# Kernel optimization log

Hardware: AMD Instinct MI355X
Metric: run time of the kernel (lower is better)

Reference implementation:

```python
import jax, jax.numpy as jnp
import numpy as np

HIDDEN = 1024
INTER = 256
N_EXPERTS = 16
B, T = 4, 2048
NEG_INF = -1000000000.0


def setup_inputs() -> dict:
    key = jax.random.key(0)
    ks = jax.random.split(key, 5)
    hidden_states = jax.random.normal(ks[0], (B, T, HIDDEN), dtype=jnp.float32)
    sim_matrix = jax.random.normal(ks[1], (HIDDEN, N_EXPERTS), dtype=jnp.float32)
    threshold = jnp.zeros((1,), dtype=jnp.float32)
    # torch Linear weights: w1 [I, C], w2 [C, I]; store per-expert stacked in
    # matmul-friendly layout: w1 [E, C, I], w2 [E, I, C]
    w1 = jax.random.normal(ks[2], (N_EXPERTS, HIDDEN, INTER), dtype=jnp.float32) / np.sqrt(HIDDEN)
    w2 = jax.random.normal(ks[3], (N_EXPERTS, INTER, HIDDEN), dtype=jnp.float32) / np.sqrt(INTER)
    return {"hidden_states": hidden_states, "sim_matrix": sim_matrix,
            "threshold": threshold, "w1": w1, "w2": w2}


def _l2norm(x, axis):
    return x / jnp.maximum(jnp.linalg.norm(x, axis=axis, keepdims=True), 1e-12)


def reference(hidden_states, sim_matrix, threshold, w1, w2):
    Bq, Tq, C = hidden_states.shape
    x = hidden_states.reshape(-1, C)                      # [N, C]
    # gate
    scores = _l2norm(x, -1) @ _l2norm(sim_matrix, 0)      # [N, E]
    activated = scores > threshold
    k_per_token = activated.sum(axis=-1)                  # [N] int
    masked = jnp.where(activated, scores, NEG_INF)
    routing_weights = jax.nn.softmax(masked, axis=-1)     # [N, E]
    # dense all-expert FFN
    h = jax.nn.gelu(jnp.einsum('nc,eci->nei', x, w1), approximate=False)
    out = jnp.einsum('nei,eic->nec', h, w2)               # [N, E, C]
    final = jnp.einsum('nec,ne->nc', out, routing_weights)
    return final.reshape(Bq, Tq, C), scores, k_per_token
```

## Files before the change

### kernel.cpp

```cpp
#include <hip/hip_runtime.h>
#include <hip/hip_bf16.h>
#include <math.h>

#define NTOK 8192
#define HID  1024
#define ISZ  256
#define NEXP 16
#define NBIG 4096

typedef __attribute__((ext_vector_type(8))) short bf16x8;
typedef __attribute__((ext_vector_type(4))) float f32x4;

__device__ __forceinline__ unsigned short f2bf(float f) {
  unsigned u = __float_as_uint(f);
  u += 0x7fff + ((u >> 16) & 1);
  return (unsigned short)(u >> 16);
}

__device__ __forceinline__ void async16(void* l, const void* g) {
  __builtin_amdgcn_global_load_lds(
      (const __attribute__((address_space(1))) unsigned int*)g,
      (__attribute__((address_space(3))) unsigned int*)l, 16, 0, 0);
}

__global__ void simnorm_kernel(const float* __restrict__ sm, float* __restrict__ inv_smn) {
  __shared__ float red[16][17];
  int t = threadIdx.x;
  int e = t & 15, g = t >> 4;
  float ss = 0.f;
  for (int c = g; c < HID; c += 16) {
    float v = sm[c * NEXP + e];
    ss += v * v;
  }
  red[e][g] = ss;
  __syncthreads();
  if (t < 16) {
    float s = 0.f;
    #pragma unroll
    for (int i = 0; i < 16; i++) s += red[t][i];
    inv_smn[t] = 1.f / fmaxf(sqrtf(s), 1e-12f);
  }
}

__global__ __launch_bounds__(256)
void gate_kernel(const float* __restrict__ x, const float* __restrict__ sm,
                 const float* __restrict__ thr, const float* __restrict__ inv_smn,
                 float* __restrict__ scores_out, float* __restrict__ k_out,
                 float* __restrict__ rw_out, unsigned short* __restrict__ xb_out) {
  const int n = blockIdx.x;
  const int t = threadIdx.x;
  const int lane = t & 63, wave = t >> 6;
  const float* xr = x + (size_t)n * HID;

  float p[16];
  #pragma unroll
  for (int e = 0; e < 16; e++) p[e] = 0.f;
  float ss = 0.f;

  #pragma unroll
  for (int q = 0; q < 4; q++) {
    int c = t + q * 256;
    float v = xr[c];
    ss += v * v;
    xb_out[(size_t)n * HID + c] = f2bf(v);
    const float4* smr = (const float4*)(sm + (size_t)c * NEXP);
    float4 s0 = smr[0], s1 = smr[1], s2 = smr[2], s3 = smr[3];
    p[0] += v * s0.x;  p[1] += v * s0.y;  p[2] += v * s0.z;  p[3] += v * s0.w;
    p[4] += v * s1.x;  p[5] += v * s1.y;  p[6] += v * s1.z;  p[7] += v * s1.w;
    p[8] += v * s2.x;  p[9] += v * s2.y;  p[10] += v * s2.z; p[11] += v * s2.w;
    p[12] += v * s3.x; p[13] += v * s3.y; p[14] += v * s3.z; p[15] += v * s3.w;
  }

  #pragma unroll
  for (int off = 32; off > 0; off >>= 1) {
    ss += __shfl_down(ss, off, 64);
    #pragma unroll
    for (int e = 0; e < 16; e++) p[e] += __shfl_down(p[e], off, 64);
  }

  __shared__ float red[4][17];
  __shared__ float sc[16];
  if (lane == 0) {
    red[wave][0] = ss;
    #pragma unroll
    for (int e = 0; e < 16; e++) red[wave][1 + e] = p[e];
  }
  __syncthreads();

  if (t < 16) {
    float d = red[0][1 + t] + red[1][1 + t] + red[2][1 + t] + red[3][1 + t];
    float ssum = red[0][0] + red[1][0] + red[2][0] + red[3][0];
    float inv_x = 1.f / fmaxf(sqrtf(ssum), 1e-12f);
    float s = d * inv_x * inv_smn[t];
    scores_out[(size_t)n * 16 + t] = s;
    sc[t] = s;
  }
  __syncthreads();

  if (t < 16) {
    float thrv = thr[0];
    float s = sc[t];
    bool act = s > thrv;
    float m = act ? s : -INFINITY;
    int cnt = act ? 1 : 0;
    #pragma unroll
    for (int off = 8; off > 0; off >>= 1) {
      m = fmaxf(m, __shfl_xor(m, off, 16));
      cnt += __shfl_xor(cnt, off, 16);
    }
    float pv;
    if (cnt > 0) pv = act ? expf(s - m) : 0.f;
    else         pv = 1.f;
    float sum = pv;
    #pragma unroll
    for (int off = 8; off > 0; off >>= 1) sum += __shfl_xor(sum, off, 16);
    rw_out[(size_t)n * 16 + t] = pv / sum;
    if (t == 0) k_out[n] = (float)cnt;
  }
}

__global__ __launch_bounds__(256)
void transpose_cast_kernel(const float* __restrict__ src, unsigned short* __restrict__ dst,
                           int R, int C, int dstride, int e_src_stride, int e_dst_mult) {
  __shared__ float tile[32][33];
  const int e = blockIdx.z;
  const int r0 = blockIdx.y * 32, c0 = blockIdx.x * 32;
  const int tx = threadIdx.x & 31, ty = threadIdx.x >> 5;
  const float* s = src + (size_t)e * e_src_stride;
  #pragma unroll
  for (int q = 0; q < 4; q++) {
    int r = r0 + ty + q * 8;
    tile[ty + q * 8][tx] = s[(size_t)r * C + c0 + tx];
  }
  __syncthreads();
  unsigned short* d = dst + (size_t)e * e_dst_mult;
  #pragma unroll
  for (int q = 0; q < 4; q++) {
    int cc = c0 + ty + q * 8;
    int r  = r0 + tx;
    d[(size_t)cc * dstride + r] = f2bf(tile[tx][ty + q * 8]);
  }
}

#define PHASE(Q, CK, SU, WAIT_)                                                       \
  {                                                                                   \
    bf16x8 afr[4], bfr[4];                                                            \
    _Pragma("unroll")                                                                 \
    for (int fm = 0; fm < 4; fm++)                                                    \
      afr[fm] = *(const bf16x8*)(bufA + (Q)*16384 + wmo + fm*2048 + lro + (CK));      \
    _Pragma("unroll")                                                                 \
    for (int fn = 0; fn < 2; fn++) {                                                  \
      bfr[fn]     = *(const bf16x8*)(bufB + wno + fn*2048 + lro + (CK));              \
      bfr[2 + fn] = *(const bf16x8*)(bufB + 16384 + wno + fn*2048 + lro + (CK));      \
    }                                                                                 \
    _Pragma("unroll")                                                                 \
    for (int i = 0; i < 2; i++) {                                                     \
      if ((SU) == 0) async16(ldsAn + o16[i],         Ag + (size_t)aRow[i]*LD + kn + aCol[i]);        \
      if ((SU) == 1) async16(ldsBn + o16[i],         Bg + (size_t)bRow[i]*LD + kn + bCol[i]);        \
      if ((SU) == 2) async16(ldsAn + 16384 + o16[i], Ag + (size_t)(aRow[i] + 64)*LD + kn + aCol[i]); \
      if ((SU) == 3) async16(ldsBn + 16384 + o16[i], Bg + (size_t)(bRow[i] + 32)*LD + kn + bCol[i]); \
    }                                                                                 \
    __builtin_amdgcn_sched_barrier(0);                                                \
    __builtin_amdgcn_s_barrier();                                                     \
    asm volatile("s_waitcnt lgkmcnt(0)" ::: "memory");                                \
    __builtin_amdgcn_sched_barrier(0);                                                \
    __builtin_amdgcn_s_setprio(1);                                                    \
    _Pragma("unroll")                                                                 \
    for (int fm = 0; fm < 4; fm++)                                                    \
      _Pragma("unroll")                                                               \
      for (int fn = 0; fn < 4; fn++)                                                  \
        acc[(Q)*4+fm][fn] = __builtin_amdgcn_mfma_f32_16x16x32_bf16(                  \
            afr[fm], bfr[fn], acc[(Q)*4+fm][fn], 0, 0, 0);                            \
    __builtin_amdgcn_s_setprio(0);                                                    \
    __builtin_amdgcn_sched_barrier(0);                                                \
    if ((WAIT_) == 4) { asm volatile("s_waitcnt vmcnt(4)" ::: "memory"); }            \
    if ((WAIT_) == 2) { asm volatile("s_waitcnt vmcnt(2)" ::: "memory"); }            \
    __builtin_amdgcn_s_barrier();                                                     \
    __builtin_amdgcn_sched_barrier(0);                                                \
  }

template <int EPI, int KEXT, int LD, int NBN, int SPLITK>
__global__ __launch_bounds__(512, 2)
void gemm256(const unsigned short* __restrict__ A, const unsigned short* __restrict__ B,
             float* __restrict__ Cf, float* __restrict__ Cf2,
             unsigned short* __restrict__ Cb, const float* __restrict__ rw) {
  __shared__ __align__(1024) char lds[131072];
  constexpr int NT = KEXT / 64;
  const int tid = threadIdx.x;
  const int lane = tid & 63, wid = tid >> 6;
  const int wm = wid >> 2, wn = wid & 3;
  const int lr = lane & 15;

  const int nwg = gridDim.x;
  const int cpx = nwg >> 3;
  int wg = (blockIdx.x & 7) * cpx + (blockIdx.x >> 3);
  int kz = 0;
  if (SPLITK == 2) { kz = wg / (nwg >> 1); wg = wg % (nwg >> 1); }
  const int bm = wg / NBN, bn = wg % NBN;

  const int swz = (lr & 7) << 4;
  const int colk0 = ((lane >> 4) * 16) ^ swz;
  const int colk1 = (64 + (lane >> 4) * 16) ^ swz;
  const int wmo = wm * 8192, wno = wn * 4096, lro = lr * 128;

  int aRow[2], aCol[2], bRow[2], bCol[2], o16[2];
  #pragma unroll
  for (int i = 0; i < 2; i++) {
    int o = (i * 512 + tid) * 16;
    o16[i] = o;
    { int wmb = o >> 13, ob = o & 8191, r = ob >> 7, cb = ob & 127;
      aRow[i] = wmb * 128 + r; aCol[i] = (cb ^ ((r & 7) << 4)) >> 1; }
    { int wnb = o >> 12, ob = o & 4095, r = ob >> 7, cb = ob & 127;
      bRow[i] = wnb * 64 + r; bCol[i] = (cb ^ ((r & 7) << 4)) >> 1; }
  }

  const unsigned short* Ag = A + (size_t)bm * 256 * LD + (size_t)kz * KEXT;
  const unsigned short* Bg = B + (size_t)bn * 256 * LD + (size_t)kz * KEXT;

  f32x4 acc[8][4];
  #pragma unroll
  for (int m = 0; m < 8; m++)
    #pragma unroll
    for (int n = 0; n < 4; n++) acc[m][n] = (f32x4){0.f, 0.f, 0.f, 0.f};

  #pragma unroll
  for (int i = 0; i < 2; i++) async16(lds + o16[i],                 Ag + (size_t)aRow[i] * LD + aCol[i]);
  #pragma unroll
  for (int i = 0; i < 2; i++) async16(lds + 65536 + o16[i],         Bg + (size_t)bRow[i] * LD + bCol[i]);
  #pragma unroll
  for (int i = 0; i < 2; i++) async16(lds + 65536 + 16384 + o16[i], Bg + (size_t)(bRow[i] + 32) * LD + bCol[i]);
  #pragma unroll
  for (int i = 0; i < 2; i++) async16(lds + 16384 + o16[i],         Ag + (size_t)(aRow[i] + 64) * LD + aCol[i]);
  asm volatile("s_waitcnt vmcnt(2)" ::: "memory");
  __builtin_amdgcn_s_barrier();

  #pragma unroll 1
  for (int t = 0; t < NT; t += 2) {
    {
      const char* bufA = lds;
      const char* bufB = lds + 65536;
      char* ldsAn = lds + 32768;
      char* ldsBn = lds + 65536 + 32768;
      const int kn = ((t + 1) & (NT - 1)) << 6;
      PHASE(0, colk0, 0, 4)
      PHASE(0, colk1, 1, 4)
      PHASE(1, colk0, 3, 0)
      PHASE(1, colk1, 2, 2)
    }
    {
      const char* bufA = lds + 32768;
      const char* bufB = lds + 65536 + 32768;
      char* ldsAn = lds;
      char* ldsBn = lds + 65536;
      const int kn = ((t + 2) & (NT - 1)) << 6;
      PHASE(0, colk0, 0, 4)
      PHASE(0, colk1, 1, 4)
      PHASE(1, colk0, 3, 0)
      PHASE(1, colk1, 2, 2)
    }
  }

  asm volatile("s_waitcnt vmcnt(0)" ::: "memory");

  const int jr = (lane >> 4) * 4;
  if (EPI == 1) {
    float wrow[8][4];
    #pragma unroll
    for (int m = 0; m < 8; m++)
      #pragma unroll
      for (int j = 0; j < 4; j++)
        wrow[m][j] = rw[(size_t)(bm * 256 + wm * 128 + m * 16 + jr + j) * 16 + bn];
    #pragma unroll
    for (int m = 0; m < 8; m++) {
      #pragma unroll
      for (int n = 0; n < 4; n++) {
        int col = bn * 256 + wn * 64 + n * 16 + lr;
        #pragma unroll
        for (int j = 0; j < 4; j++) {
          int r = bm * 256 + wm * 128 + m * 16 + jr + j;
          float v = acc[m][n][j];
          float g = 0.7978845608f * (v + 0.044715f * v * v * v);
          float e = __expf(2.f * g);
          float th = 1.f - 2.f / (e + 1.f);
          float ge = 0.5f * v * (1.f + th);
          Cb[(size_t)r * NBIG + col] = f2bf(ge * wrow[m][j]);
        }
      }
    }
  } else {
    float* cfp = (SPLITK == 2 && kz == 1) ? Cf2 : Cf;
    #pragma unroll
    for (int m = 0; m < 8; m++) {
      #pragma unroll
      for (int n = 0; n < 4; n++) {
        int col = bn * 256 + wn * 64 + n * 16 + lr;
        #pragma unroll
        for (int j = 0; j < 4; j++) {
          int r = bm * 256 + wm * 128 + m * 16 + jr + j;
          cfp[(size_t)r * HID + col] = acc[m][n][j];
        }
      }
    }
  }
}

__global__ __launch_bounds__(256)
void addk(float* __restrict__ out, const float* __restrict__ p1, int n4) {
  int i = blockIdx.x * blockDim.x + threadIdx.x;
  const int stride = gridDim.x * blockDim.x;
  for (; i < n4; i += stride) {
    float4 a = ((const float4*)out)[i];
    float4 b = ((const float4*)p1)[i];
    a.x += b.x; a.y += b.y; a.z += b.z; a.w += b.w;
    ((float4*)out)[i] = a;
  }
}

extern "C" void kernel_launch(void* const* d_in, const int* in_sizes, int n_in,
                              void* d_out, int out_size, void* d_ws, size_t ws_size,
                              hipStream_t stream) {
  const float* x   = (const float*)d_in[0];
  const float* sm  = (const float*)d_in[1];
  const float* thr = (const float*)d_in[2];
  const float* w1  = (const float*)d_in[3];
  const float* w2  = (const float*)d_in[4];

  float* out_final  = (float*)d_out;
  float* out_scores = out_final + (size_t)NTOK * HID;
  float* out_k      = out_scores + (size_t)NTOK * NEXP;

  char* ws = (char*)d_ws;
  size_t off = 0;
  float* inv_smn = (float*)(ws + off); off += 256;
  float* rwbuf   = (float*)(ws + off); off += (size_t)NTOK * NEXP * 4;
  unsigned short* Xb  = (unsigned short*)(ws + off); off += (size_t)NTOK * HID * 2;
  unsigned short* W1T = (unsigned short*)(ws + off); off += (size_t)NBIG * HID * 2;
  unsigned short* W2T = (unsigned short*)(ws + off); off += (size_t)HID * NBIG * 2;
  unsigned short* H   = (unsigned short*)(ws + off); off += (size_t)NTOK * NBIG * 2;
  float* P1 = (float*)(ws + off);
  const bool split = ws_size >= off + (size_t)NTOK * HID * 4;

  simnorm_kernel<<<1, 256, 0, stream>>>(sm, inv_smn);
  gate_kernel<<<NTOK, 256, 0, stream>>>(x, sm, thr, inv_smn, out_scores, out_k, rwbuf, Xb);
  transpose_cast_kernel<<<dim3(ISZ / 32, HID / 32, NEXP), 256, 0, stream>>>(
      w1, W1T, HID, ISZ, HID, HID * ISZ, ISZ * HID);
  transpose_cast_kernel<<<dim3(HID / 32, ISZ / 32, NEXP), 256, 0, stream>>>(
      w2, W2T, ISZ, HID, NBIG, ISZ * HID, ISZ);

  gemm256<1, HID, HID, 16, 1><<<512, 512, 0, stream>>>(Xb, W1T, nullptr, nullptr, H, rwbuf);

  if (split) {
    gemm256<2, NBIG / 2, NBIG, 4, 2><<<256, 512, 0, stream>>>(H, W2T, out_final, P1, nullptr, nullptr);
    addk<<<2048, 256, 0, stream>>>(out_final, P1, NTOK * HID / 4);
  } else {
    gemm256<2, NBIG, NBIG, 4, 1><<<128, 512, 0, stream>>>(H, W2T, out_final, nullptr, nullptr, nullptr);
  }
}
```

Before: 236.0 us.

## Replace split-K second GEMM with 128x256 tiled kernel and simplify pipeline phases

```diff
diff --git a/kernel.cpp b/kernel.cpp
--- a/kernel.cpp
+++ b/kernel.cpp
@@ -142,47 +142,49 @@
   }
 }
 
-#define PHASE(Q, CK, SU, WAIT_)                                                       \
-  {                                                                                   \
-    bf16x8 afr[4], bfr[4];                                                            \
-    _Pragma("unroll")                                                                 \
-    for (int fm = 0; fm < 4; fm++)                                                    \
-      afr[fm] = *(const bf16x8*)(bufA + (Q)*16384 + wmo + fm*2048 + lro + (CK));      \
-    _Pragma("unroll")                                                                 \
-    for (int fn = 0; fn < 2; fn++) {                                                  \
-      bfr[fn]     = *(const bf16x8*)(bufB + wno + fn*2048 + lro + (CK));              \
-      bfr[2 + fn] = *(const bf16x8*)(bufB + 16384 + wno + fn*2048 + lro + (CK));      \
-    }                                                                                 \
-    _Pragma("unroll")                                                                 \
-    for (int i = 0; i < 2; i++) {                                                     \
-      if ((SU) == 0) async16(ldsAn + o16[i],         Ag + (size_t)aRow[i]*LD + kn + aCol[i]);        \
-      if ((SU) == 1) async16(ldsBn + o16[i],         Bg + (size_t)bRow[i]*LD + kn + bCol[i]);        \
-      if ((SU) == 2) async16(ldsAn + 16384 + o16[i], Ag + (size_t)(aRow[i] + 64)*LD + kn + aCol[i]); \
-      if ((SU) == 3) async16(ldsBn + 16384 + o16[i], Bg + (size_t)(bRow[i] + 32)*LD + kn + bCol[i]); \
-    }                                                                                 \
-    __builtin_amdgcn_sched_barrier(0);                                                \
-    __builtin_amdgcn_s_barrier();                                                     \
-    asm volatile("s_waitcnt lgkmcnt(0)" ::: "memory");                                \
-    __builtin_amdgcn_sched_barrier(0);                                                \
-    __builtin_amdgcn_s_setprio(1);                                                    \
-    _Pragma("unroll")                                                                 \
-    for (int fm = 0; fm < 4; fm++)                                                    \
-      _Pragma("unroll")                                                               \
-      for (int fn = 0; fn < 4; fn++)                                                  \
-        acc[(Q)*4+fm][fn] = __builtin_amdgcn_mfma_f32_16x16x32_bf16(                  \
-            afr[fm], bfr[fn], acc[(Q)*4+fm][fn], 0, 0, 0);                            \
-    __builtin_amdgcn_s_setprio(0);                                                    \
-    __builtin_amdgcn_sched_barrier(0);                                                \
-    if ((WAIT_) == 4) { asm volatile("s_waitcnt vmcnt(4)" ::: "memory"); }            \
-    if ((WAIT_) == 2) { asm volatile("s_waitcnt vmcnt(2)" ::: "memory"); }            \
-    __builtin_amdgcn_s_barrier();                                                     \
-    __builtin_amdgcn_sched_barrier(0);                                                \
-  }
-
-template <int EPI, int KEXT, int LD, int NBN, int SPLITK>
+#define G1PHASE(CK, STG, WAIT_)                                                \
+  {                                                                            \
+    bf16x8 afr[8], bfr[4];                                                     \
+    _Pragma("unroll")                                                          \
+    for (int q = 0; q < 2; q++)                                                \
+      _Pragma("unroll")                                                        \
+      for (int ml = 0; ml < 4; ml++)                                           \
+        afr[q*4+ml] = *(const bf16x8*)(bufA + q*16384 + wmo + ml*2048 + lro + (CK)); \
+    _Pragma("unroll")                                                          \
+    for (int qn = 0; qn < 2; qn++)                                             \
+      _Pragma("unroll")                                                        \
+      for (int nl = 0; nl < 2; nl++)                                           \
+        bfr[qn*2+nl] = *(const bf16x8*)(bufB + qn*16384 + wno + nl*2048 + lro + (CK)); \
+    if (STG) {                                                                 \
+      _Pragma("unroll")                                                        \
+      for (int i = 0; i < 2; i++) {                                            \
+        async16(ldsAn + o16[i],         Ag + (size_t)aRow[i]*LD + kn + aCol[i]);      \
+        async16(ldsBn + o16[i],         Bg + (size_t)bRow[i]*LD + kn + bCol[i]);      \
+        async16(ldsBn + 16384 + o16[i], Bg + (size_t)(bRow[i]+32)*LD + kn + bCol[i]); \
+        async16(ldsAn + 16384 + o16[i], Ag + (size_t)(aRow[i]+64)*LD + kn + aCol[i]); \
+      }                                                                        \
+    }                                                                          \
+    __builtin_amdgcn_sched_barrier(0);                                         \
+    __builtin_amdgcn_s_barrier();                                              \
+    asm volatile("s_waitcnt lgkmcnt(0)" ::: "memory");                         \
+    __builtin_amdgcn_sched_barrier(0);                                         \
+    __builtin_amdgcn_s_setprio(1);                                             \
+    _Pragma("unroll")                                                          \
+    for (int m8 = 0; m8 < 8; m8++)                                             \
+      _Pragma("unroll")                                                        \
+      for (int n4 = 0; n4 < 4; n4++)                                           \
+        acc[m8][n4] = __builtin_amdgcn_mfma_f32_16x16x32_bf16(                 \
+            afr[m8], bfr[n4], acc[m8][n4], 0, 0, 0);                           \
+    __builtin_amdgcn_s_setprio(0);                                             \
+    __builtin_amdgcn_sched_barrier(0);                                         \
+    if (WAIT_) { asm volatile("s_waitcnt vmcnt(0)" ::: "memory"); }            \
+    __builtin_amdgcn_s_barrier();                                              \
+    __builtin_amdgcn_sched_barrier(0);                                         \
+  }
+
+template <int KEXT, int LD, int NBN>
 __global__ __launch_bounds__(512, 2)
-void gemm256(const unsigned short* __restrict__ A, const unsigned short* __restrict__ B,
-             float* __restrict__ Cf, float* __restrict__ Cf2,
+void gemm1_k(const unsigned short* __restrict__ A, const unsigned short* __restrict__ B,
              unsigned short* __restrict__ Cb, const float* __restrict__ rw) {
   __shared__ __align__(1024) char lds[131072];
   constexpr int NT = KEXT / 64;
@@ -194,8 +196,6 @@
   const int nwg = gridDim.x;
   const int cpx = nwg >> 3;
   int wg = (blockIdx.x & 7) * cpx + (blockIdx.x >> 3);
-  int kz = 0;
-  if (SPLITK == 2) { kz = wg / (nwg >> 1); wg = wg % (nwg >> 1); }
   const int bm = wg / NBN, bn = wg % NBN;
 
   const int swz = (lr & 7) << 4;
@@ -214,8 +214,8 @@
       bRow[i] = wnb * 64 + r; bCol[i] = (cb ^ ((r & 7) << 4)) >> 1; }
   }
 
-  const unsigned short* Ag = A + (size_t)bm * 256 * LD + (size_t)kz * KEXT;
-  const unsigned short* Bg = B + (size_t)bn * 256 * LD + (size_t)kz * KEXT;
+  const unsigned short* Ag = A + (size_t)bm * 256 * LD;
+  const unsigned short* Bg = B + (size_t)bn * 256 * LD;
 
   f32x4 acc[8][4];
   #pragma unroll
@@ -231,7 +231,7 @@
   for (int i = 0; i < 2; i++) async16(lds + 65536 + 16384 + o16[i], Bg + (size_t)(bRow[i] + 32) * LD + bCol[i]);
   #pragma unroll
   for (int i = 0; i < 2; i++) async16(lds + 16384 + o16[i],         Ag + (size_t)(aRow[i] + 64) * LD + aCol[i]);
-  asm volatile("s_waitcnt vmcnt(2)" ::: "memory");
+  asm volatile("s_waitcnt vmcnt(0)" ::: "memory");
   __builtin_amdgcn_s_barrier();
 
   #pragma unroll 1
@@ -242,10 +242,8 @@
       char* ldsAn = lds + 32768;
       char* ldsBn = lds + 65536 + 32768;
       const int kn = ((t + 1) & (NT - 1)) << 6;
-      PHASE(0, colk0, 0, 4)
-      PHASE(0, colk1, 1, 4)
-      PHASE(1, colk0, 3, 0)
-      PHASE(1, colk1, 2, 2)
+      G1PHASE(colk0, 1, 0)
+      G1PHASE(colk1, 0, 1)
     }
     {
       const char* bufA = lds + 32768;
@@ -253,66 +251,162 @@
       char* ldsAn = lds;
       char* ldsBn = lds + 65536;
       const int kn = ((t + 2) & (NT - 1)) << 6;
-      PHASE(0, colk0, 0, 4)
-      PHASE(0, colk1, 1, 4)
-      PHASE(1, colk0, 3, 0)
-      PHASE(1, colk1, 2, 2)
+      G1PHASE(colk0, 1, 0)
+      G1PHASE(colk1, 0, 1)
     }
   }
 
   asm volatile("s_waitcnt vmcnt(0)" ::: "memory");
 
   const int jr = (lane >> 4) * 4;
-  if (EPI == 1) {
-    float wrow[8][4];
-    #pragma unroll
-    for (int m = 0; m < 8; m++)
+  float wrow[8][4];
+  #pragma unroll
+  for (int m = 0; m < 8; m++)
+    #pragma unroll
+    for (int j = 0; j < 4; j++)
+      wrow[m][j] = rw[(size_t)(bm * 256 + wm * 128 + m * 16 + jr + j) * 16 + bn];
+  #pragma unroll
+  for (int m = 0; m < 8; m++) {
+    #pragma unroll
+    for (int n = 0; n < 4; n++) {
+      int col = bn * 256 + wn * 64 + n * 16 + lr;
       #pragma unroll
-      for (int j = 0; j < 4; j++)
-        wrow[m][j] = rw[(size_t)(bm * 256 + wm * 128 + m * 16 + jr + j) * 16 + bn];
-    #pragma unroll
-    for (int m = 0; m < 8; m++) {
+      for (int j = 0; j < 4; j++) {
+        int r = bm * 256 + wm * 128 + m * 16 + jr + j;
+        float v = acc[m][n][j];
+        float g = 0.7978845608f * (v + 0.044715f * v * v * v);
+        float e = __expf(2.f * g);
+        float th = 1.f - 2.f / (e + 1.f);
+        float ge = 0.5f * v * (1.f + th);
+        Cb[(size_t)r * NBIG + col] = f2bf(ge * wrow[m][j]);
+      }
+    }
+  }
+}
+
+#define G2PHASE(CK, STG, WAIT_)                                                \
+  {                                                                            \
+    bf16x8 afr[4], bfr[4];                                                     \
+    _Pragma("unroll")                                                          \
+    for (int ml = 0; ml < 4; ml++)                                             \
+      afr[ml] = *(const bf16x8*)(bufA + wmo + ml*2048 + lro + (CK));           \
+    _Pragma("unroll")                                                          \
+    for (int nl = 0; nl < 4; nl++)                                             \
+      bfr[nl] = *(const bf16x8*)(bufB + wno + nl*2048 + lro + (CK));           \
+    if (STG) {                                                                 \
+      _Pragma("unroll")                                                        \
+      for (int i = 0; i < 2; i++)                                              \
+        async16(ldsAn + o16[i], Ag + (size_t)aRow[i]*K + kn + aCol[i]);        \
+      _Pragma("unroll")                                                        \
+      for (int i = 0; i < 4; i++)                                              \
+        async16(ldsBn + o16b[i], Bg + (size_t)bRow[i]*K + kn + bCol[i]);       \
+    }                                                                          \
+    __builtin_amdgcn_sched_barrier(0);                                         \
+    __builtin_amdgcn_s_barrier();                                              \
+    asm volatile("s_waitcnt lgkmcnt(0)" ::: "memory");                         \
+    __builtin_amdgcn_sched_barrier(0);                                         \
+    __builtin_amdgcn_s_setprio(1);                                             \
+    _Pragma("unroll")                                                          \
+    for (int m4 = 0; m4 < 4; m4++)                                             \
+      _Pragma("unroll")                                                        \
+      for (int n4 = 0; n4 < 4; n4++)                                           \
+        acc[m4][n4] = __builtin_amdgcn_mfma_f32_16x16x32_bf16(                 \
+            afr[m4], bfr[n4], acc[m4][n4], 0, 0, 0);                           \
+    __builtin_amdgcn_s_setprio(0);                                             \
+    __builtin_amdgcn_sched_barrier(0);                                         \
+    if (WAIT_) { asm volatile("s_waitcnt vmcnt(0)" ::: "memory"); }            \
+    __builtin_amdgcn_s_barrier();                                              \
+    __builtin_amdgcn_sched_barrier(0);                                         \
+  }
+
+template <int K>
+__global__ __launch_bounds__(512, 2)
+void gemm2_k(const unsigned short* __restrict__ A, const unsigned short* __restrict__ B,
+             float* __restrict__ Cf) {
+  __shared__ __align__(1024) char lds[98304];
+  constexpr int NT = K / 64;
+  const int tid = threadIdx.x;
+  const int lane = tid & 63, wid = tid >> 6;
+  const int wm = wid >> 2, wn = wid & 3;
+  const int lr = lane & 15;
+
+  const int wg = (blockIdx.x & 7) * 32 + (blockIdx.x >> 3);
+  const int bm = wg >> 2, bn = wg & 3;
+
+  const int swz = (lr & 7) << 4;
+  const int colk0 = ((lane >> 4) * 16) ^ swz;
+  const int colk1 = (64 + (lane >> 4) * 16) ^ swz;
+  const int wmo = wm * 8192, wno = wn * 8192, lro = lr * 128;
+
+  int aRow[2], aCol[2], o16[2];
+  int bRow[4], bCol[4], o16b[4];
+  #pragma unroll
+  for (int i = 0; i < 2; i++) {
+    int o = (i * 512 + tid) * 16;
+    o16[i] = o;
+    int r = o >> 7, cb = o & 127;
+    aRow[i] = r; aCol[i] = (cb ^ ((r & 7) << 4)) >> 1;
+  }
+  #pragma unroll
+  for (int i = 0; i < 4; i++) {
+    int o = (i * 512 + tid) * 16;
+    o16b[i] = o;
+    int r = o >> 7, cb = o & 127;
+    bRow[i] = r; bCol[i] = (cb ^ ((r & 7) << 4)) >> 1;
+  }
+
+  const unsigned short* Ag = A + (size_t)bm * 128 * K;
+  const unsigned short* Bg = B + (size_t)bn * 256 * K;
+
+  f32x4 acc[4][4];
+  #pragma unroll
+  for (int m = 0; m < 4; m++)
+    #pragma unroll
+    for (int n = 0; n < 4; n++) acc[m][n] = (f32x4){0.f, 0.f, 0.f, 0.f};
+
+  #pragma unroll
+  for (int i = 0; i < 2; i++) async16(lds + o16[i],          Ag + (size_t)aRow[i] * K + aCol[i]);
+  #pragma unroll
+  for (int i = 0; i < 4; i++) async16(lds + 32768 + o16b[i], Bg + (size_t)bRow[i] * K + bCol[i]);
+  asm volatile("s_waitcnt vmcnt(0)" ::: "memory");
+  __builtin_amdgcn_s_barrier();
+
+  #pragma unroll 1
+  for (int t = 0; t < NT; t += 2) {
+    {
+      const char* bufA = lds;
+      const char* bufB = lds + 32768;
+      char* ldsAn = lds + 16384;
+      char* ldsBn = lds + 32768 + 32768;
+      const int kn = ((t + 1) & (NT - 1)) << 6;
+      G2PHASE(colk0, 1, 0)
+      G2PHASE(colk1, 0, 1)
+    }
+    {
+      const char* bufA = lds + 16384;
+      const char* bufB = lds + 32768 + 32768;
+      char* ldsAn = lds;
+      char* ldsBn = lds + 32768;
+      const int kn = ((t + 2) & (NT - 1)) << 6;
+      G2PHASE(colk0, 1, 0)
+      G2PHASE(colk1, 0, 1)
+    }
+  }
+
+  asm volatile("s_waitcnt vmcnt(0)" ::: "memory");
+
+  const int jr = (lane >> 4) * 4;
+  #pragma unroll
+  for (int m = 0; m < 4; m++) {
+    #pragma unroll
+    for (int n = 0; n < 4; n++) {
+      int col = bn * 256 + wn * 64 + n * 16 + lr;
       #pragma unroll
-      for (int n = 0; n < 4; n++) {
-        int col = bn * 256 + wn * 64 + n * 16 + lr;
-        #pragma unroll
-        for (int j = 0; j < 4; j++) {
-          int r = bm * 256 + wm * 128 + m * 16 + jr + j;
-          float v = acc[m][n][j];
-          float g = 0.7978845608f * (v + 0.044715f * v * v * v);
-          float e = __expf(2.f * g);
-          float th = 1.f - 2.f / (e + 1.f);
-          float ge = 0.5f * v * (1.f + th);
-          Cb[(size_t)r * NBIG + col] = f2bf(ge * wrow[m][j]);
-        }
+      for (int j = 0; j < 4; j++) {
+        int r = bm * 128 + wm * 64 + m * 16 + jr + j;
+        Cf[(size_t)r * HID + col] = acc[m][n][j];
       }
     }
-  } else {
-    float* cfp = (SPLITK == 2 && kz == 1) ? Cf2 : Cf;
-    #pragma unroll
-    for (int m = 0; m < 8; m++) {
-      #pragma unroll
-      for (int n = 0; n < 4; n++) {
-        int col = bn * 256 + wn * 64 + n * 16 + lr;
-        #pragma unroll
-        for (int j = 0; j < 4; j++) {
-          int r = bm * 256 + wm * 128 + m * 16 + jr + j;
-          cfp[(size_t)r * HID + col] = acc[m][n][j];
-        }
-      }
-    }
-  }
-}
-
-__global__ __launch_bounds__(256)
-void addk(float* __restrict__ out, const float* __restrict__ p1, int n4) {
-  int i = blockIdx.x * blockDim.x + threadIdx.x;
-  const int stride = gridDim.x * blockDim.x;
-  for (; i < n4; i += stride) {
-    float4 a = ((const float4*)out)[i];
-    float4 b = ((const float4*)p1)[i];
-    a.x += b.x; a.y += b.y; a.z += b.z; a.w += b.w;
-    ((float4*)out)[i] = a;
   }
 }
 
@@ -337,8 +431,6 @@
   unsigned short* W1T = (unsigned short*)(ws + off); off += (size_t)NBIG * HID * 2;
   unsigned short* W2T = (unsigned short*)(ws + off); off += (size_t)HID * NBIG * 2;
   unsigned short* H   = (unsigned short*)(ws + off); off += (size_t)NTOK * NBIG * 2;
-  float* P1 = (float*)(ws + off);
-  const bool split = ws_size >= off + (size_t)NTOK * HID * 4;
 
   simnorm_kernel<<<1, 256, 0, stream>>>(sm, inv_smn);
   gate_kernel<<<NTOK, 256, 0, stream>>>(x, sm, thr, inv_smn, out_scores, out_k, rwbuf, Xb);
@@ -347,12 +439,6 @@
   transpose_cast_kernel<<<dim3(HID / 32, ISZ / 32, NEXP), 256, 0, stream>>>(
       w2, W2T, ISZ, HID, NBIG, ISZ * HID, ISZ);
 
-  gemm256<1, HID, HID, 16, 1><<<512, 512, 0, stream>>>(Xb, W1T, nullptr, nullptr, H, rwbuf);
-
-  if (split) {
-    gemm256<2, NBIG / 2, NBIG, 4, 2><<<256, 512, 0, stream>>>(H, W2T, out_final, P1, nullptr, nullptr);
-    addk<<<2048, 256, 0, stream>>>(out_final, P1, NTOK * HID / 4);
-  } else {
-    gemm256<2, NBIG, NBIG, 4, 1><<<128, 512, 0, stream>>>(H, W2T, out_final, nullptr, nullptr, nullptr);
-  }
-}
+  gemm1_k<HID, HID, 16><<<512, 512, 0, stream>>>(Xb, W1T, H, rwbuf);
+  gemm2_k<NBIG><<<256, 512, 0, stream>>>(H, W2T, out_final);
+}
```

Measured after the change: 221.0 us. -6.4%, faster.

## Replace fine-grained 4-phase GEMM pipeline with one barrier per K-tile

Applied to the files above, without the earlier changes.

```diff
diff --git a/kernel.cpp b/kernel.cpp
--- a/kernel.cpp
+++ b/kernel.cpp
@@ -10,6 +10,8 @@
 
 typedef __attribute__((ext_vector_type(8))) short bf16x8;
 typedef __attribute__((ext_vector_type(4))) float f32x4;
+
+#define MFMA16(a, b, c) __builtin_amdgcn_mfma_f32_16x16x32_bf16(a, b, c, 0, 0, 0)
 
 __device__ __forceinline__ unsigned short f2bf(float f) {
   unsigned u = __float_as_uint(f);
@@ -142,39 +144,37 @@
   }
 }
 
-#define PHASE(Q, CK, SU, WAIT_)                                                       \
+#define GTILE(CA, CB, NA, NB, kn)                                                     \
   {                                                                                   \
-    bf16x8 afr[4], bfr[4];                                                            \
     _Pragma("unroll")                                                                 \
-    for (int fm = 0; fm < 4; fm++)                                                    \
-      afr[fm] = *(const bf16x8*)(bufA + (Q)*16384 + wmo + fm*2048 + lro + (CK));      \
-    _Pragma("unroll")                                                                 \
-    for (int fn = 0; fn < 2; fn++) {                                                  \
-      bfr[fn]     = *(const bf16x8*)(bufB + wno + fn*2048 + lro + (CK));              \
-      bfr[2 + fn] = *(const bf16x8*)(bufB + 16384 + wno + fn*2048 + lro + (CK));      \
+    for (int i = 0; i < 2; i++) {                                                     \
+      async16((NA) + o16[i],         Ag + (size_t)aRow[i] * LD + (kn) + aCol[i]);     \
+      async16((NB) + o16[i],         Bg + (size_t)bRow[i] * LD + (kn) + bCol[i]);     \
+      async16((NA) + 16384 + o16[i], Ag + (size_t)(aRow[i] + 64) * LD + (kn) + aCol[i]); \
+      async16((NB) + 16384 + o16[i], Bg + (size_t)(bRow[i] + 32) * LD + (kn) + bCol[i]); \
     }                                                                                 \
     _Pragma("unroll")                                                                 \
-    for (int i = 0; i < 2; i++) {                                                     \
-      if ((SU) == 0) async16(ldsAn + o16[i],         Ag + (size_t)aRow[i]*LD + kn + aCol[i]);        \
-      if ((SU) == 1) async16(ldsBn + o16[i],         Bg + (size_t)bRow[i]*LD + kn + bCol[i]);        \
-      if ((SU) == 2) async16(ldsAn + 16384 + o16[i], Ag + (size_t)(aRow[i] + 64)*LD + kn + aCol[i]); \
-      if ((SU) == 3) async16(ldsBn + 16384 + o16[i], Bg + (size_t)(bRow[i] + 32)*LD + kn + bCol[i]); \
+    for (int kk = 0; kk < 2; kk++) {                                                  \
+      const int ck = kk ? colk1 : colk0;                                              \
+      bf16x8 a[8], b[4];                                                              \
+      _Pragma("unroll")                                                               \
+      for (int q = 0; q < 2; q++)                                                     \
+        _Pragma("unroll")                                                             \
+        for (int ml = 0; ml < 4; ml++)                                                \
+          a[q * 4 + ml] = *(const bf16x8*)((CA) + q * 16384 + wmo + ml * 2048 + lro + ck); \
+      _Pragma("unroll")                                                               \
+      for (int qn = 0; qn < 2; qn++)                                                  \
+        _Pragma("unroll")                                                             \
+        for (int nl = 0; nl < 2; nl++)                                                \
+          b[qn * 2 + nl] = *(const bf16x8*)((CB) + qn * 16384 + wno + nl * 2048 + lro + ck); \
+      _Pragma("unroll")                                                               \
+      for (int m8 = 0; m8 < 8; m8++)                                                  \
+        _Pragma("unroll")                                                             \
+        for (int n4 = 0; n4 < 4; n4++)                                                \
+          acc[m8][n4] = MFMA16(a[m8], b[n4], acc[m8][n4]);                            \
     }                                                                                 \
     __builtin_amdgcn_sched_barrier(0);                                                \
-    __builtin_amdgcn_s_barrier();                                                     \
-    asm volatile("s_waitcnt lgkmcnt(0)" ::: "memory");                                \
-    __builtin_amdgcn_sched_barrier(0);                                                \
-    __builtin_amdgcn_s_setprio(1);                                                    \
-    _Pragma("unroll")                                                                 \
-    for (int fm = 0; fm < 4; fm++)                                                    \
-      _Pragma("unroll")                                                               \
-      for (int fn = 0; fn < 4; fn++)                                                  \
-        acc[(Q)*4+fm][fn] = __builtin_amdgcn_mfma_f32_16x16x32_bf16(                  \
-            afr[fm], bfr[fn], acc[(Q)*4+fm][fn], 0, 0, 0);                            \
-    __builtin_amdgcn_s_setprio(0);                                                    \
-    __builtin_amdgcn_sched_barrier(0);                                                \
-    if ((WAIT_) == 4) { asm volatile("s_waitcnt vmcnt(4)" ::: "memory"); }            \
-    if ((WAIT_) == 2) { asm volatile("s_waitcnt vmcnt(2)" ::: "memory"); }            \
+    asm volatile("s_waitcnt vmcnt(0)" ::: "memory");                                  \
     __builtin_amdgcn_s_barrier();                                                     \
     __builtin_amdgcn_sched_barrier(0);                                                \
   }
@@ -224,40 +224,22 @@
     for (int n = 0; n < 4; n++) acc[m][n] = (f32x4){0.f, 0.f, 0.f, 0.f};
 
   #pragma unroll
-  for (int i = 0; i < 2; i++) async16(lds + o16[i],                 Ag + (size_t)aRow[i] * LD + aCol[i]);
-  #pragma unroll
-  for (int i = 0; i < 2; i++) async16(lds + 65536 + o16[i],         Bg + (size_t)bRow[i] * LD + bCol[i]);
-  #pragma unroll
-  for (int i = 0; i < 2; i++) async16(lds + 65536 + 16384 + o16[i], Bg + (size_t)(bRow[i] + 32) * LD + bCol[i]);
-  #pragma unroll
-  for (int i = 0; i < 2; i++) async16(lds + 16384 + o16[i],         Ag + (size_t)(aRow[i] + 64) * LD + aCol[i]);
-  asm volatile("s_waitcnt vmcnt(2)" ::: "memory");
+  for (int i = 0; i < 2; i++) {
+    async16(lds + o16[i],                 Ag + (size_t)aRow[i] * LD + aCol[i]);
+    async16(lds + 65536 + o16[i],         Bg + (size_t)bRow[i] * LD + bCol[i]);
+    async16(lds + 16384 + o16[i],         Ag + (size_t)(aRow[i] + 64) * LD + aCol[i]);
+    async16(lds + 65536 + 16384 + o16[i], Bg + (size_t)(bRow[i] + 32) * LD + bCol[i]);
+  }
+  asm volatile("s_waitcnt vmcnt(0)" ::: "memory");
   __builtin_amdgcn_s_barrier();
+  __builtin_amdgcn_sched_barrier(0);
 
   #pragma unroll 1
   for (int t = 0; t < NT; t += 2) {
-    {
-      const char* bufA = lds;
-      const char* bufB = lds + 65536;
-      char* ldsAn = lds + 32768;
-      char* ldsBn = lds + 65536 + 32768;
-      const int kn = ((t + 1) & (NT - 1)) << 6;
-      PHASE(0, colk0, 0, 4)
-      PHASE(0, colk1, 1, 4)
-      PHASE(1, colk0, 3, 0)
-      PHASE(1, colk1, 2, 2)
-    }
-    {
-      const char* bufA = lds + 32768;
-      const char* bufB = lds + 65536 + 32768;
-      char* ldsAn = lds;
-      char* ldsBn = lds + 65536;
-      const int kn = ((t + 2) & (NT - 1)) << 6;
-      PHASE(0, colk0, 0, 4)
-      PHASE(0, colk1, 1, 4)
-      PHASE(1, colk0, 3, 0)
-      PHASE(1, colk1, 2, 2)
-    }
+    GTILE(lds,         lds + 65536,         lds + 32768, lds + 65536 + 32768,
+          ((t + 1) & (NT - 1)) << 6)
+    GTILE(lds + 32768, lds + 65536 + 32768, lds,         lds + 65536,
+          ((t + 2) & (NT - 1)) << 6)
   }
 
   asm volatile("s_waitcnt vmcnt(0)" ::: "memory");
```

Result: no change. 235.8 us (-0.1%).
